# Kernel tuning notes

Hardware: AMD Instinct MI355X
Metric: run time of the kernel (lower is better)

The kernel has to match this reference:

```python
import jax, jax.numpy as jnp
import numpy as np
from jax import lax

B = 32768  # number of 5x5 patches processed in a batch
NUM_MID = 6  # middle 25->25 conv layers (layers 1..6 of 8)
NUM_W = 6    # predicted kernel weights per pixel


def _conv(x, w, b, pad):
    # x: [B,C,H,W], w: [O,I,kh,kw]
    y = lax.conv_general_dilated(x, w, (1, 1), pad,
                                 dimension_numbers=('NCHW', 'OIHW', 'NCHW'))
    return y + b[None, :, None, None]


def setup_inputs() -> dict:
    key = jax.random.key(0)
    ks = jax.random.split(key, 10)
    s = 0.1
    inp = {
        'input': jax.random.normal(ks[0], (B, 8, 5, 5), dtype=jnp.float32),
        'w0': jax.random.normal(ks[1], (25, 8, 3, 3), dtype=jnp.float32) * s,
        'b0': jax.random.normal(ks[2], (25,), dtype=jnp.float32) * s,
        'wmid': jax.random.normal(ks[3], (NUM_MID, 25, 25, 3, 3), dtype=jnp.float32) * s,
        'bmid': jax.random.normal(ks[4], (NUM_MID, 25), dtype=jnp.float32) * s,
        'wlast': jax.random.normal(ks[5], (NUM_W, 25, 3, 3), dtype=jnp.float32) * s,
        'blast': jax.random.normal(ks[6], (NUM_W,), dtype=jnp.float32) * s,
        'wpost': jax.random.normal(ks[7], (3 * NUM_W, 3, 5, 5), dtype=jnp.float32) * s,
        'bpost': jax.random.normal(ks[8], (3 * NUM_W,), dtype=jnp.float32) * s,
    }
    return inp


def reference(input, w0, b0, wmid, bmid, wlast, blast, wpost, bpost):
    # 8-layer tiny CNN predicting per-pixel softmax weights over NUM_W kernels
    h = jax.nn.relu(_conv(input, w0, b0, 'SAME'))
    for i in range(NUM_MID):  # fixed small layer count
        h = jax.nn.relu(_conv(h, wmid[i], bmid[i], 'SAME'))
    h = _conv(h, wlast, blast, 'SAME')            # [B, NUM_W, 5, 5]
    norm_w = jax.nn.softmax(h, axis=1)            # softmax over weight channels
    # postconv: 5x5 valid conv on first 3 channels -> [B, 3*NUM_W, 1, 1] -> [B,3,NUM_W]
    colors = _conv(input[:, 0:3], wpost, bpost, 'VALID').reshape(B, 3, NUM_W)
    # per-pixel matmul: filtered[:,y,x] = colors @ norm_w[:,y,x]
    filtered = jnp.einsum('bcw,bwyx->bcyx', colors, norm_w)  # [B,3,5,5]
    return filtered
```

## Files before the change

kernel.cpp:

```cpp
#include <hip/hip_runtime.h>
#include <hip/hip_bf16.h>
#include <stdint.h>


typedef short bf16x8 __attribute__((ext_vector_type(8)));
typedef float f32x4  __attribute__((ext_vector_type(4)));

#define WSB_N     73728
#define WSB_EMB   6144
#define WSF_BYTE  147456
#define WSF_BALL  0
#define WSF_BP32  256

#define L_STAGE_STRIDE 136
#define L_INPK   6800
#define L_COLB   12944
#define L_POOL   14096
#define SMB_STRIDE 98

__device__ __forceinline__ float b2f(unsigned short u) {
  union { unsigned int u; float f; } v; v.u = ((unsigned int)u) << 16; return v.f;
}
__device__ __forceinline__ unsigned short f2b(float f) {
  union { float f; unsigned int u; } v; v.f = f;
  unsigned int r = v.u + 0x7fffu + ((v.u >> 16) & 1u);
  return (unsigned short)(r >> 16);
}
__device__ __forceinline__ unsigned int pk2(float lo, float hi) {
  __hip_bfloat162 h = __float22bfloat162_rn(make_float2(lo, hi));
  union { __hip_bfloat162 h; unsigned int u; } v; v.h = h; return v.u;
}
__device__ __forceinline__ bool sniff_is_f32(const void* w0raw) {
  const unsigned short* q = (const unsigned short*)w0raw;
  int hits = 0;
  #pragma unroll
  for (int i = 0; i < 64; ++i) {
    unsigned int e = (q[i] >> 7) & 0xFFu;
    if (e >= 130u) ++hits;
  }
  return hits > 0;
}
__device__ __forceinline__ float ldw(const void* p, long idx, bool f32) {
  return f32 ? ((const float*)p)[idx] : b2f(((const unsigned short*)p)[idx]);
}
__device__ __forceinline__ int kperm(int m) {
  return (m < 16) ? ((m >> 2) * 8 + (m & 3))
                  : (((m - 16) >> 2) * 8 + 4 + (m & 3));
}

__global__ void prep_weights(const void* __restrict__ w0,
                             const void* __restrict__ b0,
                             const void* __restrict__ wm,
                             const void* __restrict__ bm,
                             const void* __restrict__ wl,
                             const void* __restrict__ bl,
                             const void* __restrict__ wp,
                             const void* __restrict__ bp,
                             unsigned short* __restrict__ wsb,
                             float* __restrict__ wsf) {
  const bool f32 = sniff_is_f32(w0);
  int e = blockIdx.x * blockDim.x + threadIdx.x;
  if (e < WSB_N) {
    int l = e / 9216, r = e % 9216, t = r / 1024, r2 = r % 1024;
    int o = r2 >> 5, c = r2 & 31;
    if (l == 7 && o >= 6) return;
    float v = 0.f;
    if (l < 7) {
      int co = kperm(o);
      if (co < 25) {
        if (l == 0) { if (c < 8)  v = ldw(w0, (co * 8 + c) * 9 + t, f32); }
        else        { if (c < 25) v = ldw(wm, (((l - 1) * 25 + co) * 25 + c) * 9 + t, f32); }
      }
    } else {
      if (c < 25) v = ldw(wl, (o * 25 + c) * 9 + t, f32);
    }
    wsb[e] = f2b(v);
  } else if (e < WSB_N + WSB_EMB) {
    int idx = e - WSB_N;
    int hl = idx / 3072, rem = idx % 3072;
    int chunk = rem / 1024, r2 = rem % 1024;
    int o = r2 >> 5, k = r2 & 31;
    float w = (o < 18 && k < 25) ? ldw(wp, (o * 3 + chunk) * 25 + k, f32) : 0.f;
    unsigned short hi = f2b(w);
    unsigned short val = hl ? f2b(w - b2f(hi)) : hi;
    int rowidx = hl * 96 + chunk * 32 + o;
    int t = rowidx / 26, rr = 6 + rowidx % 26;
    wsb[7 * 9216 + t * 1024 + rr * 32 + k] = val;
  } else {
    int q = e - WSB_N - WSB_EMB;
    if (q < 256) {
      int l = q >> 5, m = q & 31;
      float v = 0.f;
      if (l < 7) {
        int co = kperm(m);
        if (co < 25) v = (l == 0) ? ldw(b0, co, f32) : ldw(bm, (l - 1) * 25 + co, f32);
      } else {
        if (m < 6) v = ldw(bl, m, f32);
      }
      wsf[WSF_BALL + q] = v;
    } else if (q < 288) {
      int oc = q - 256;
      wsf[WSF_BP32 + oc] = (oc < 18) ? ldw(bp, oc, f32) : 0.f;
    }
  }
}

__global__ __launch_bounds__(64)
__attribute__((amdgpu_waves_per_eu(2, 2)))
void pcnn_mfma(
    const void* __restrict__ inp,
    const void* __restrict__ w0raw,
    const unsigned short* __restrict__ wsb,
    const float* __restrict__ wsf,
    void* __restrict__ out) {
  __shared__ __align__(16) unsigned char pool[L_POOL];
  short* stage = (short*)pool;
  short* inpk  = (short*)(pool + L_INPK);
  float* colb  = (float*)(pool + L_COLB);
  float* smb   = (float*)pool;

  const bool f32m = sniff_is_f32(w0raw);
  const int lane = threadIdx.x;
  const int col  = lane & 15;
  const int quad = lane >> 4;
  const long g   = blockIdx.x;

  bf16x8 WC[2][3][2];
  #pragma unroll
  for (int hl = 0; hl < 2; ++hl)
    #pragma unroll
    for (int ch = 0; ch < 3; ++ch)
      #pragma unroll
      for (int hf = 0; hf < 2; ++hf) {
        const int rowidx = hl * 96 + ch * 32 + hf * 16 + col;
        const int t = rowidx / 26, rr = 6 + rowidx % 26;
        WC[hl][ch][hf] = *(const bf16x8*)(wsb + 7 * 9216 + t * 1024 + rr * 32 + quad * 8);
      }
  f32x4 c0 = *(const f32x4*)(wsf + WSF_BP32 + quad * 4);
  f32x4 c1 = *(const f32x4*)(wsf + WSF_BP32 + 16 + quad * 4);

  for (int i = lane; i < 672; i += 64) {
    int s = 25 + i % 7, rest = i / 7;
    inpk[rest * 32 + s] = 0;
  }

  #pragma unroll 1
  for (int c0i = 0; c0i < 3200; c0i += 1600) {
    float v[25];
    #pragma unroll
    for (int j = 0; j < 25; ++j)
      v[j] = ldw(inp, g * 3200 + c0i + j * 64 + lane, f32m);
    #pragma unroll
    for (int j = 0; j < 25; ++j) {
      const int e = c0i + j * 64 + lane;
      int b = e / 200, r = e % 200, c = r / 25, px = r % 25;
      unsigned short hi = f2b(v[j]);
      stage[px * L_STAGE_STRIDE + b * 8 + c] = hi;
      if (c < 3) {
        inpk[((0 * 3 + c) * 16 + b) * 32 + px] = hi;
        inpk[((1 * 3 + c) * 16 + b) * 32 + px] = f2b(v[j] - b2f(hi));
      }
    }
  }
  __asm__ volatile("s_waitcnt lgkmcnt(0)" ::: "memory");

  #pragma unroll
  for (int ch = 0; ch < 3; ++ch) {
    bf16x8 Bhi = *(const bf16x8*)(inpk + ((0 * 3 + ch) * 16 + col) * 32 + quad * 8);
    bf16x8 Blo = *(const bf16x8*)(inpk + ((1 * 3 + ch) * 16 + col) * 32 + quad * 8);
    c0 = __builtin_amdgcn_mfma_f32_16x16x32_bf16(WC[0][ch][0], Bhi, c0, 0, 0, 0);
    c0 = __builtin_amdgcn_mfma_f32_16x16x32_bf16(WC[0][ch][0], Blo, c0, 0, 0, 0);
    c0 = __builtin_amdgcn_mfma_f32_16x16x32_bf16(WC[1][ch][0], Bhi, c0, 0, 0, 0);
    c1 = __builtin_amdgcn_mfma_f32_16x16x32_bf16(WC[0][ch][1], Bhi, c1, 0, 0, 0);
    c1 = __builtin_amdgcn_mfma_f32_16x16x32_bf16(WC[0][ch][1], Blo, c1, 0, 0, 0);
    c1 = __builtin_amdgcn_mfma_f32_16x16x32_bf16(WC[1][ch][1], Bhi, c1, 0, 0, 0);
  }
  #pragma unroll
  for (int r = 0; r < 4; ++r) colb[col * 18 + quad * 4 + r] = c0[r];
  if (quad == 0) { colb[col * 18 + 16] = c1[0]; colb[col * 18 + 17] = c1[1]; }

  bf16x8 X[25], Y[25];
  #pragma unroll
  for (int p = 0; p < 25; ++p) {
    union { bf16x8 v; uint4 q4; } t;
    t.q4 = make_uint4(0u, 0u, 0u, 0u);
    if (quad == 0) t.q4 = *(const uint4*)(stage + p * L_STAGE_STRIDE + col * 8);
    X[p] = t.v;
  }

  auto conv = [&](const bf16x8 (&in)[25], bf16x8 (&outp)[25], int l) {
    const unsigned short* WA = wsb + l * 9216;
    bf16x8 A0[9], A1[9];
    #pragma unroll
    for (int t = 0; t < 9; ++t) {
      A0[t] = *(const bf16x8*)(WA + t * 1024 + col * 32 + quad * 8);
      A1[t] = *(const bf16x8*)(WA + t * 1024 + (16 + col) * 32 + quad * 8);
    }
    const f32x4 bias0 = *(const f32x4*)(wsf + WSF_BALL + l * 32 + quad * 4);
    const f32x4 bias1 = *(const f32x4*)(wsf + WSF_BALL + l * 32 + 16 + quad * 4);
    f32x4 p0e, p0o, p1e, p1o;
    #pragma unroll
    for (int p = 0; p < 25; ++p) {
      const int py = p / 5, pxx = p % 5;
      f32x4 a0e = bias0, a1e = bias1;
      f32x4 a0o = {0.f, 0.f, 0.f, 0.f}, a1o = {0.f, 0.f, 0.f, 0.f};
      #pragma unroll
      for (int dy = -1; dy <= 1; ++dy)
        #pragma unroll
        for (int dx = -1; dx <= 1; ++dx)
          if ((unsigned)(py + dy) < 5u && (unsigned)(pxx + dx) < 5u) {
            const int t = (dy + 1) * 3 + (dx + 1);
            const int q = p + dy * 5 + dx;
            if (t & 1) {
              a0o = __builtin_amdgcn_mfma_f32_16x16x32_bf16(A0[t], in[q], a0o, 0, 0, 0);
              a1o = __builtin_amdgcn_mfma_f32_16x16x32_bf16(A1[t], in[q], a1o, 0, 0, 0);
            } else {
              a0e = __builtin_amdgcn_mfma_f32_16x16x32_bf16(A0[t], in[q], a0e, 0, 0, 0);
              a1e = __builtin_amdgcn_mfma_f32_16x16x32_bf16(A1[t], in[q], a1e, 0, 0, 0);
            }
          }
      if (p > 0) {
        union { bf16x8 v; unsigned int uu[4]; } nb;
        nb.uu[0] = pk2(fmaxf(p0e[0] + p0o[0], 0.f), fmaxf(p0e[1] + p0o[1], 0.f));
        nb.uu[1] = pk2(fmaxf(p0e[2] + p0o[2], 0.f), fmaxf(p0e[3] + p0o[3], 0.f));
        nb.uu[2] = pk2(fmaxf(p1e[0] + p1o[0], 0.f), fmaxf(p1e[1] + p1o[1], 0.f));
        nb.uu[3] = pk2(fmaxf(p1e[2] + p1o[2], 0.f), fmaxf(p1e[3] + p1o[3], 0.f));
        outp[p - 1] = nb.v;
      }
      p0e = a0e; p0o = a0o; p1e = a1e; p1o = a1o;
    }
    {
      union { bf16x8 v; unsigned int uu[4]; } nb;
      nb.uu[0] = pk2(fmaxf(p0e[0] + p0o[0], 0.f), fmaxf(p0e[1] + p0o[1], 0.f));
      nb.uu[1] = pk2(fmaxf(p0e[2] + p0o[2], 0.f), fmaxf(p0e[3] + p0o[3], 0.f));
      nb.uu[2] = pk2(fmaxf(p1e[0] + p1o[0], 0.f), fmaxf(p1e[1] + p1o[1], 0.f));
      nb.uu[3] = pk2(fmaxf(p1e[2] + p1o[2], 0.f), fmaxf(p1e[3] + p1o[3], 0.f));
      outp[24] = nb.v;
    }
  };

  conv(X, Y, 0);
  #pragma unroll 1
  for (int i = 0; i < 3; ++i) {
    conv(Y, X, 2 * i + 1);
    conv(X, Y, 2 * i + 2);
  }

  {
    const unsigned short* WA = wsb + 7 * 9216;
    bf16x8 A[9];
    #pragma unroll
    for (int t = 0; t < 9; ++t)
      A[t] = *(const bf16x8*)(WA + t * 1024 + col * 32 + quad * 8);
    const f32x4 biasl = *(const f32x4*)(wsf + WSF_BALL + 7 * 32 + quad * 4);
    f32x4 pa;
    auto tail = [&](const f32x4& a, int p) {
      float l4 = __shfl_xor(a[0], 16);
      float l5 = __shfl_xor(a[1], 16);
      if (quad == 0) {
        float m = fmaxf(fmaxf(fmaxf(a[0], a[1]), fmaxf(a[2], a[3])), fmaxf(l4, l5));
        float e0 = __expf(a[0] - m), e1 = __expf(a[1] - m), e2 = __expf(a[2] - m);
        float e3 = __expf(a[3] - m), e4 = __expf(l4 - m), e5 = __expf(l5 - m);
        float inv = 1.f / (e0 + e1 + e2 + e3 + e4 + e5);
        float* sp = smb + p * SMB_STRIDE + col * 6;
        sp[0] = e0 * inv; sp[1] = e1 * inv; sp[2] = e2 * inv;
        sp[3] = e3 * inv; sp[4] = e4 * inv; sp[5] = e5 * inv;
      }
    };
    #pragma unroll
    for (int p = 0; p < 25; ++p) {
      const int py = p / 5, pxx = p % 5;
      f32x4 ae = biasl, ao = {0.f, 0.f, 0.f, 0.f};
      #pragma unroll
      for (int dy = -1; dy <= 1; ++dy)
        #pragma unroll
        for (int dx = -1; dx <= 1; ++dx)
          if ((unsigned)(py + dy) < 5u && (unsigned)(pxx + dx) < 5u) {
            const int t = (dy + 1) * 3 + (dx + 1);
            const int q = p + dy * 5 + dx;
            if (t & 1)
              ao = __builtin_amdgcn_mfma_f32_16x16x32_bf16(A[t], Y[q], ao, 0, 0, 0);
            else
              ae = __builtin_amdgcn_mfma_f32_16x16x32_bf16(A[t], Y[q], ae, 0, 0, 0);
          }
      if (p > 0) tail(pa, p - 1);
      f32x4 a;
      a[0] = ae[0] + ao[0]; a[1] = ae[1] + ao[1];
      a[2] = ae[2] + ao[2]; a[3] = ae[3] + ao[3];
      pa = a;
    }
    tail(pa, 24);
  }
  __asm__ volatile("s_waitcnt lgkmcnt(0)" ::: "memory");

  for (int e = lane; e < 1200; e += 64) {
    int b = e / 75, r = e % 75, c = r / 25, p = r % 25;
    float v = 0.f;
    #pragma unroll
    for (int w = 0; w < 6; ++w)
      v = fmaf(colb[b * 18 + c * 6 + w], smb[p * SMB_STRIDE + b * 6 + w], v);
    const long oidx = g * 1200 + e;
    if (f32m) ((float*)out)[oidx] = v;
    else      ((unsigned short*)out)[oidx] = f2b(v);
  }
}

extern "C" void kernel_launch(void* const* d_in, const int* in_sizes, int n_in,
                              void* d_out, int out_size, void* d_ws, size_t ws_size,
                              hipStream_t stream) {
  unsigned short* wsb = (unsigned short*)d_ws;
  float* wsf = (float*)((char*)d_ws + WSF_BYTE);
  const int B = in_sizes[0] / 200;

  const int prep_n = WSB_N + WSB_EMB + 288;
  prep_weights<<<(prep_n + 255) / 256, 256, 0, stream>>>(
      d_in[1], d_in[2], d_in[3], d_in[4], d_in[5], d_in[6], d_in[7], d_in[8],
      wsb, wsf);
  pcnn_mfma<<<B / 16, 64, 0, stream>>>(d_in[0], d_in[1], wsb, wsf, d_out);
}
```

Before: 157.0 us.

## Split output channels across two waves with LDS exchange per conv layer

Each block now runs two wavefronts. Each wave computes 16 of the 32 output channels per conv layer, and the full activation is exchanged through shared memory with barriers between layers. The last layer splits pixels across the waves. The aim is to halve per-wave MFMA work and register pressure (only one activation array and 9 weight fragments) so more waves fit per SIMD. The cost is two block barriers per layer, extra LDS round-trips, and more shared memory per block.

```diff
diff --git a/kernel.cpp b/kernel.cpp
--- a/kernel.cpp
+++ b/kernel.cpp
@@ -14,8 +14,8 @@
 
 #define L_STAGE_STRIDE 136
 #define L_INPK   6800
-#define L_COLB   12944
-#define L_POOL   14096
+#define L_COLB   25600
+#define L_POOL   26752
 #define SMB_STRIDE 98
 
 __device__ __forceinline__ float b2f(unsigned short u) {
@@ -105,8 +105,8 @@
   }
 }
 
-__global__ __launch_bounds__(64)
-__attribute__((amdgpu_waves_per_eu(2, 2)))
+__global__ __launch_bounds__(128)
+__attribute__((amdgpu_waves_per_eu(3)))
 void pcnn_mfma(
     const void* __restrict__ inp,
     const void* __restrict__ w0raw,
@@ -116,43 +116,42 @@
   __shared__ __align__(16) unsigned char pool[L_POOL];
   short* stage = (short*)pool;
   short* inpk  = (short*)(pool + L_INPK);
+  short* YL    = (short*)pool;
   float* colb  = (float*)(pool + L_COLB);
   float* smb   = (float*)pool;
 
   const bool f32m = sniff_is_f32(w0raw);
-  const int lane = threadIdx.x;
+  const int tid  = threadIdx.x;
+  const int lane = tid & 63;
+  const int wid  = tid >> 6;
   const int col  = lane & 15;
   const int quad = lane >> 4;
   const long g   = blockIdx.x;
 
-  bf16x8 WC[2][3][2];
+  bf16x8 WC[2][3];
   #pragma unroll
   for (int hl = 0; hl < 2; ++hl)
     #pragma unroll
-    for (int ch = 0; ch < 3; ++ch)
-      #pragma unroll
-      for (int hf = 0; hf < 2; ++hf) {
-        const int rowidx = hl * 96 + ch * 32 + hf * 16 + col;
-        const int t = rowidx / 26, rr = 6 + rowidx % 26;
-        WC[hl][ch][hf] = *(const bf16x8*)(wsb + 7 * 9216 + t * 1024 + rr * 32 + quad * 8);
-      }
-  f32x4 c0 = *(const f32x4*)(wsf + WSF_BP32 + quad * 4);
-  f32x4 c1 = *(const f32x4*)(wsf + WSF_BP32 + 16 + quad * 4);
-
-  for (int i = lane; i < 672; i += 64) {
+    for (int ch = 0; ch < 3; ++ch) {
+      const int rowidx = hl * 96 + ch * 32 + wid * 16 + col;
+      const int t = rowidx / 26, rr = 6 + rowidx % 26;
+      WC[hl][ch] = *(const bf16x8*)(wsb + 7 * 9216 + t * 1024 + rr * 32 + quad * 8);
+    }
+  f32x4 cacc = *(const f32x4*)(wsf + WSF_BP32 + wid * 16 + quad * 4);
+
+  for (int i = tid; i < 672; i += 128) {
     int s = 25 + i % 7, rest = i / 7;
     inpk[rest * 32 + s] = 0;
   }
 
-  #pragma unroll 1
-  for (int c0i = 0; c0i < 3200; c0i += 1600) {
+  {
     float v[25];
     #pragma unroll
     for (int j = 0; j < 25; ++j)
-      v[j] = ldw(inp, g * 3200 + c0i + j * 64 + lane, f32m);
+      v[j] = ldw(inp, g * 3200 + j * 128 + tid, f32m);
     #pragma unroll
     for (int j = 0; j < 25; ++j) {
-      const int e = c0i + j * 64 + lane;
+      const int e = j * 128 + tid;
       int b = e / 200, r = e % 200, c = r / 25, px = r % 25;
       unsigned short hi = f2b(v[j]);
       stage[px * L_STAGE_STRIDE + b * 8 + c] = hi;
@@ -162,24 +161,25 @@
       }
     }
   }
-  __asm__ volatile("s_waitcnt lgkmcnt(0)" ::: "memory");
+  __syncthreads();
 
   #pragma unroll
   for (int ch = 0; ch < 3; ++ch) {
     bf16x8 Bhi = *(const bf16x8*)(inpk + ((0 * 3 + ch) * 16 + col) * 32 + quad * 8);
     bf16x8 Blo = *(const bf16x8*)(inpk + ((1 * 3 + ch) * 16 + col) * 32 + quad * 8);
-    c0 = __builtin_amdgcn_mfma_f32_16x16x32_bf16(WC[0][ch][0], Bhi, c0, 0, 0, 0);
-    c0 = __builtin_amdgcn_mfma_f32_16x16x32_bf16(WC[0][ch][0], Blo, c0, 0, 0, 0);
-    c0 = __builtin_amdgcn_mfma_f32_16x16x32_bf16(WC[1][ch][0], Bhi, c0, 0, 0, 0);
-    c1 = __builtin_amdgcn_mfma_f32_16x16x32_bf16(WC[0][ch][1], Bhi, c1, 0, 0, 0);
-    c1 = __builtin_amdgcn_mfma_f32_16x16x32_bf16(WC[0][ch][1], Blo, c1, 0, 0, 0);
-    c1 = __builtin_amdgcn_mfma_f32_16x16x32_bf16(WC[1][ch][1], Bhi, c1, 0, 0, 0);
-  }
-  #pragma unroll
-  for (int r = 0; r < 4; ++r) colb[col * 18 + quad * 4 + r] = c0[r];
-  if (quad == 0) { colb[col * 18 + 16] = c1[0]; colb[col * 18 + 17] = c1[1]; }
-
-  bf16x8 X[25], Y[25];
+    cacc = __builtin_amdgcn_mfma_f32_16x16x32_bf16(WC[0][ch], Bhi, cacc, 0, 0, 0);
+    cacc = __builtin_amdgcn_mfma_f32_16x16x32_bf16(WC[0][ch], Blo, cacc, 0, 0, 0);
+    cacc = __builtin_amdgcn_mfma_f32_16x16x32_bf16(WC[1][ch], Bhi, cacc, 0, 0, 0);
+  }
+  if (wid == 0) {
+    #pragma unroll
+    for (int r = 0; r < 4; ++r) colb[col * 18 + quad * 4 + r] = cacc[r];
+  } else if (quad == 0) {
+    colb[col * 18 + 16] = cacc[0];
+    colb[col * 18 + 17] = cacc[1];
+  }
+
+  bf16x8 X[25];
   #pragma unroll
   for (int p = 0; p < 25; ++p) {
     union { bf16x8 v; uint4 q4; } t;
@@ -187,23 +187,20 @@
     if (quad == 0) t.q4 = *(const uint4*)(stage + p * L_STAGE_STRIDE + col * 8);
     X[p] = t.v;
   }
-
-  auto conv = [&](const bf16x8 (&in)[25], bf16x8 (&outp)[25], int l) {
+  __syncthreads();
+
+  #pragma unroll 1
+  for (int l = 0; l < 7; ++l) {
     const unsigned short* WA = wsb + l * 9216;
-    bf16x8 A0[9], A1[9];
-    #pragma unroll
-    for (int t = 0; t < 9; ++t) {
-      A0[t] = *(const bf16x8*)(WA + t * 1024 + col * 32 + quad * 8);
-      A1[t] = *(const bf16x8*)(WA + t * 1024 + (16 + col) * 32 + quad * 8);
-    }
-    const f32x4 bias0 = *(const f32x4*)(wsf + WSF_BALL + l * 32 + quad * 4);
-    const f32x4 bias1 = *(const f32x4*)(wsf + WSF_BALL + l * 32 + 16 + quad * 4);
-    f32x4 p0e, p0o, p1e, p1o;
+    bf16x8 A[9];
+    #pragma unroll
+    for (int t = 0; t < 9; ++t)
+      A[t] = *(const bf16x8*)(WA + t * 1024 + (wid * 16 + col) * 32 + quad * 8);
+    const f32x4 bias = *(const f32x4*)(wsf + WSF_BALL + l * 32 + wid * 16 + quad * 4);
     #pragma unroll
     for (int p = 0; p < 25; ++p) {
       const int py = p / 5, pxx = p % 5;
-      f32x4 a0e = bias0, a1e = bias1;
-      f32x4 a0o = {0.f, 0.f, 0.f, 0.f}, a1o = {0.f, 0.f, 0.f, 0.f};
+      f32x4 ae = bias, ao = {0.f, 0.f, 0.f, 0.f};
       #pragma unroll
       for (int dy = -1; dy <= 1; ++dy)
         #pragma unroll
@@ -211,39 +208,21 @@
           if ((unsigned)(py + dy) < 5u && (unsigned)(pxx + dx) < 5u) {
             const int t = (dy + 1) * 3 + (dx + 1);
             const int q = p + dy * 5 + dx;
-            if (t & 1) {
-              a0o = __builtin_amdgcn_mfma_f32_16x16x32_bf16(A0[t], in[q], a0o, 0, 0, 0);
-              a1o = __builtin_amdgcn_mfma_f32_16x16x32_bf16(A1[t], in[q], a1o, 0, 0, 0);
-            } else {
-              a0e = __builtin_amdgcn_mfma_f32_16x16x32_bf16(A0[t], in[q], a0e, 0, 0, 0);
-              a1e = __builtin_amdgcn_mfma_f32_16x16x32_bf16(A1[t], in[q], a1e, 0, 0, 0);
-            }
+            if (t & 1)
+              ao = __builtin_amdgcn_mfma_f32_16x16x32_bf16(A[t], X[q], ao, 0, 0, 0);
+            else
+              ae = __builtin_amdgcn_mfma_f32_16x16x32_bf16(A[t], X[q], ae, 0, 0, 0);
           }
-      if (p > 0) {
-        union { bf16x8 v; unsigned int uu[4]; } nb;
-        nb.uu[0] = pk2(fmaxf(p0e[0] + p0o[0], 0.f), fmaxf(p0e[1] + p0o[1], 0.f));
-        nb.uu[1] = pk2(fmaxf(p0e[2] + p0o[2], 0.f), fmaxf(p0e[3] + p0o[3], 0.f));
-        nb.uu[2] = pk2(fmaxf(p1e[0] + p1o[0], 0.f), fmaxf(p1e[1] + p1o[1], 0.f));
-        nb.uu[3] = pk2(fmaxf(p1e[2] + p1o[2], 0.f), fmaxf(p1e[3] + p1o[3], 0.f));
-        outp[p - 1] = nb.v;
-      }
-      p0e = a0e; p0o = a0o; p1e = a1e; p1o = a1o;
-    }
-    {
-      union { bf16x8 v; unsigned int uu[4]; } nb;
-      nb.uu[0] = pk2(fmaxf(p0e[0] + p0o[0], 0.f), fmaxf(p0e[1] + p0o[1], 0.f));
-      nb.uu[1] = pk2(fmaxf(p0e[2] + p0o[2], 0.f), fmaxf(p0e[3] + p0o[3], 0.f));
-      nb.uu[2] = pk2(fmaxf(p1e[0] + p1o[0], 0.f), fmaxf(p1e[1] + p1o[1], 0.f));
-      nb.uu[3] = pk2(fmaxf(p1e[2] + p1o[2], 0.f), fmaxf(p1e[3] + p1o[3], 0.f));
-      outp[24] = nb.v;
-    }
-  };
-
-  conv(X, Y, 0);
-  #pragma unroll 1
-  for (int i = 0; i < 3; ++i) {
-    conv(Y, X, 2 * i + 1);
-    conv(X, Y, 2 * i + 2);
+      union { uint2 u2; unsigned int uu[2]; } w2;
+      w2.uu[0] = pk2(fmaxf(ae[0] + ao[0], 0.f), fmaxf(ae[1] + ao[1], 0.f));
+      w2.uu[1] = pk2(fmaxf(ae[2] + ao[2], 0.f), fmaxf(ae[3] + ao[3], 0.f));
+      *(uint2*)(YL + p * 512 + col * 32 + quad * 8 + wid * 4) = w2.u2;
+    }
+    __syncthreads();
+    #pragma unroll
+    for (int p = 0; p < 25; ++p)
+      X[p] = *(const bf16x8*)(YL + p * 512 + col * 32 + quad * 8);
+    __syncthreads();
   }
 
   {
@@ -253,8 +232,26 @@
     for (int t = 0; t < 9; ++t)
       A[t] = *(const bf16x8*)(WA + t * 1024 + col * 32 + quad * 8);
     const f32x4 biasl = *(const f32x4*)(wsf + WSF_BALL + 7 * 32 + quad * 4);
-    f32x4 pa;
-    auto tail = [&](const f32x4& a, int p) {
+    #pragma unroll
+    for (int p = 0; p < 25; ++p) {
+      if ((p < 13) != (wid == 0)) continue;
+      const int py = p / 5, pxx = p % 5;
+      f32x4 ae = biasl, ao = {0.f, 0.f, 0.f, 0.f};
+      #pragma unroll
+      for (int dy = -1; dy <= 1; ++dy)
+        #pragma unroll
+        for (int dx = -1; dx <= 1; ++dx)
+          if ((unsigned)(py + dy) < 5u && (unsigned)(pxx + dx) < 5u) {
+            const int t = (dy + 1) * 3 + (dx + 1);
+            const int q = p + dy * 5 + dx;
+            if (t & 1)
+              ao = __builtin_amdgcn_mfma_f32_16x16x32_bf16(A[t], X[q], ao, 0, 0, 0);
+            else
+              ae = __builtin_amdgcn_mfma_f32_16x16x32_bf16(A[t], X[q], ae, 0, 0, 0);
+          }
+      f32x4 a;
+      a[0] = ae[0] + ao[0]; a[1] = ae[1] + ao[1];
+      a[2] = ae[2] + ao[2]; a[3] = ae[3] + ao[3];
       float l4 = __shfl_xor(a[0], 16);
       float l5 = __shfl_xor(a[1], 16);
       if (quad == 0) {
@@ -266,34 +263,11 @@
         sp[0] = e0 * inv; sp[1] = e1 * inv; sp[2] = e2 * inv;
         sp[3] = e3 * inv; sp[4] = e4 * inv; sp[5] = e5 * inv;
       }
-    };
-    #pragma unroll
-    for (int p = 0; p < 25; ++p) {
-      const int py = p / 5, pxx = p % 5;
-      f32x4 ae = biasl, ao = {0.f, 0.f, 0.f, 0.f};
-      #pragma unroll
-      for (int dy = -1; dy <= 1; ++dy)
-        #pragma unroll
-        for (int dx = -1; dx <= 1; ++dx)
-          if ((unsigned)(py + dy) < 5u && (unsigned)(pxx + dx) < 5u) {
-            const int t = (dy + 1) * 3 + (dx + 1);
-            const int q = p + dy * 5 + dx;
-            if (t & 1)
-              ao = __builtin_amdgcn_mfma_f32_16x16x32_bf16(A[t], Y[q], ao, 0, 0, 0);
-            else
-              ae = __builtin_amdgcn_mfma_f32_16x16x32_bf16(A[t], Y[q], ae, 0, 0, 0);
-          }
-      if (p > 0) tail(pa, p - 1);
-      f32x4 a;
-      a[0] = ae[0] + ao[0]; a[1] = ae[1] + ao[1];
-      a[2] = ae[2] + ao[2]; a[3] = ae[3] + ao[3];
-      pa = a;
-    }
-    tail(pa, 24);
-  }
-  __asm__ volatile("s_waitcnt lgkmcnt(0)" ::: "memory");
-
-  for (int e = lane; e < 1200; e += 64) {
+    }
+  }
+  __syncthreads();
+
+  for (int e = tid; e < 1200; e += 128) {
     int b = e / 75, r = e % 75, c = r / 25, p = r % 25;
     float v = 0.f;
     #pragma unroll
@@ -316,5 +290,5 @@
   prep_weights<<<(prep_n + 255) / 256, 256, 0, stream>>>(
       d_in[1], d_in[2], d_in[3], d_in[4], d_in[5], d_in[6], d_in[7], d_in[8],
       wsb, wsf);
-  pcnn_mfma<<<B / 16, 64, 0, stream>>>(d_in[0], d_in[1], wsb, wsf, d_out);
-}
+  pcnn_mfma<<<B / 16, 128, 0, stream>>>(d_in[0], d_in[1], wsb, wsf, d_out);
+}
```

Result: slower. 174.3 us (+11.0%).
